# Kernel optimization log

Measured on AMD Instinct MI355X. Metric: run time of the kernel, lower is better.

Reference implementation:

```python
import jax, jax.numpy as jnp
import numpy as np


def _gru_layer(x, W_ih, W_hh, b_ih, b_hh):
    # x: [B, T, in]; W_ih: [3H, in]; W_hh: [3H, H]; gate order (r, z, n) as in PyTorch.
    B, T, _ = x.shape
    H = W_hh.shape[1]
    # Precompute input-side gate pre-activations for the whole sequence (batched GEMM).
    gi = jnp.einsum('bti,gi->btg', x, W_ih) + b_ih  # [B, T, 3H]

    def step(h, gi_t):
        gh = h @ W_hh.T + b_hh                      # [B, 3H]
        i_r, i_z, i_n = jnp.split(gi_t, 3, axis=-1)
        h_r, h_z, h_n = jnp.split(gh, 3, axis=-1)
        r = jax.nn.sigmoid(i_r + h_r)
        z = jax.nn.sigmoid(i_z + h_z)
        n = jnp.tanh(i_n + r * h_n)
        h_new = (1.0 - z) * n + z * h
        return h_new, h_new

    h0 = jnp.zeros((B, H), x.dtype)
    _, hs = jax.lax.scan(step, h0, jnp.swapaxes(gi, 0, 1))  # hs: [T, B, H]
    return jnp.swapaxes(hs, 0, 1)                            # [B, T, H]


def setup_inputs() -> dict:
    key = jax.random.key(0)
    ks = jax.random.split(key, 11)
    B, T, I, H, O = 512, 512, 64, 128, 1
    s = 0.1  # keep gate pre-activations out of saturation
    return {
        'x':     jax.random.normal(ks[0], (B, T, I), jnp.float32),
        'W_ih0': jax.random.normal(ks[1], (3 * H, I), jnp.float32) * s,
        'W_hh0': jax.random.normal(ks[2], (3 * H, H), jnp.float32) * s,
        'b_ih0': jax.random.normal(ks[3], (3 * H,), jnp.float32) * s,
        'b_hh0': jax.random.normal(ks[4], (3 * H,), jnp.float32) * s,
        'W_ih1': jax.random.normal(ks[5], (3 * H, H), jnp.float32) * s,
        'W_hh1': jax.random.normal(ks[6], (3 * H, H), jnp.float32) * s,
        'b_ih1': jax.random.normal(ks[7], (3 * H,), jnp.float32) * s,
        'b_hh1': jax.random.normal(ks[8], (3 * H,), jnp.float32) * s,
        'W_fc':  jax.random.normal(ks[9], (O, H), jnp.float32) * s,
        'b_fc':  jax.random.normal(ks[10], (O,), jnp.float32) * s,
    }


def reference(x, W_ih0, W_hh0, b_ih0, b_hh0, W_ih1, W_hh1, b_ih1, b_hh1, W_fc, b_fc):
    h1 = _gru_layer(x, W_ih0, W_hh0, b_ih0, b_hh0)   # [B, T, H]
    h2 = _gru_layer(h1, W_ih1, W_hh1, b_ih1, b_hh1)  # [B, T, H]
    return h2[:, -1, :] @ W_fc.T + b_fc               # [B, O]
```

## Files before the change

kernel.cpp:

```cpp
#include <hip/hip_runtime.h>
#include <stdint.h>

typedef __bf16 bf16x8 __attribute__((ext_vector_type(8)));
typedef float  floatx4 __attribute__((ext_vector_type(4)));
typedef int    i32x4  __attribute__((ext_vector_type(4)));

#define T_LEN 512
#define BT    4
#define NTHR  1024
#define XS    72
#define HIS   144
#define HFS   132

#if __has_builtin(__builtin_amdgcn_exp2f)
#define EXP2(x) __builtin_amdgcn_exp2f(x)
#else
#define EXP2(x) exp2f(x)
#endif

#define MFMA_BF(a,b,c)  __builtin_amdgcn_mfma_f32_16x16x32_bf16((a),(b),(c),0,0,0)
#define MFMA_I8(a,b,c)  __builtin_amdgcn_mfma_i32_16x16x64_i8((a),(b),(c),0,0,0)

#define BARRIER_LDS() asm volatile("s_waitcnt lgkmcnt(0)\n\ts_barrier" ::: "memory")

#define L2E   1.4426950408889634f
#define S_RZ  (-L2E / (254.f * 127.f))
#define S_N   (-2.f * L2E / (254.f * 127.f))

__device__ __forceinline__ float rcpf(float x) { return __builtin_amdgcn_rcpf(x); }

__device__ __forceinline__ bf16x8 wfrag_bf(const float* W, int ldk, int row, int k0, float scale) {
    const float* p = W + (size_t)row * ldk + k0;
    bf16x8 r;
    #pragma unroll
    for (int j = 0; j < 8; ++j) r[j] = (__bf16)(p[j] * scale);
    return r;
}
__device__ __forceinline__ i32x4 wfrag_i8(const float* W, int ldk, int row, int k0) {
    const float* p = W + (size_t)row * ldk + k0;
    i32x4 r;
    #pragma unroll
    for (int d = 0; d < 4; ++d) {
        uint32_t dw = 0;
        #pragma unroll
        for (int j = 0; j < 4; ++j) {
            float q = __builtin_rintf(p[d * 4 + j] * 254.f);
            q = fminf(127.f, fmaxf(-127.f, q));
            dw |= ((uint32_t)((int)q & 0xff)) << (8 * j);
        }
        r[d] = (int)dw;
    }
    return r;
}

__global__ __launch_bounds__(NTHR, 4) void gru_fused(
    const float* __restrict__ x,
    const float* __restrict__ Wih0, const float* __restrict__ Whh0,
    const float* __restrict__ bih0, const float* __restrict__ bhh0,
    const float* __restrict__ Wih1, const float* __restrict__ Whh1,
    const float* __restrict__ bih1, const float* __restrict__ bhh1,
    const float* __restrict__ Wfc,  const float* __restrict__ bfc,
    float* __restrict__ out)
{
    __shared__ __align__(16) __bf16      xb[2][16 * XS];
    __shared__ __align__(16) signed char h0i[2][16 * HIS];
    __shared__ __align__(16) signed char h1i[2][16 * HIS];
    __shared__ __align__(16) float       hfin[16 * HFS];

    const int tid  = threadIdx.x;
    const int lane = tid & 63;
    const int ln16 = lane & 15;
    const int quad = lane >> 4;
    const int q8   = quad * 8;
    const int q16  = quad * 16;
    const int wave = tid >> 6;
    const int brow = blockIdx.x * BT;

    for (int i = tid; i < 16 * HIS; i += NTHR) {
        h0i[0][i] = 0; h0i[1][i] = 0;
        h1i[0][i] = 0; h1i[1][i] = 0;
    }
    for (int i = tid; i < 16 * XS; i += NTHR) {
        xb[0][i] = (__bf16)0.f; xb[1][i] = (__bf16)0.f;
    }
    __syncthreads();

    if (wave < 8) {
        const int wv = wave;
        const int c  = wv * 16 + ln16;
        const float bNi = -2.f * L2E * bih0[256 + c];
        const float bNh = -2.f * L2E * bhh0[256 + c];
        const float bR  = -L2E * (bih0[c] + bhh0[c]);
        const float bZ  = -L2E * (bih0[128 + c] + bhh0[128 + c]);
        bf16x8 wI[3][2];
        i32x4  wH[3][2];
        #pragma unroll
        for (int g = 0; g < 3; ++g) {
            const int row = g * 128 + c;
            const float sc = (g == 2) ? (-2.f * L2E) : (-L2E);
            #pragma unroll
            for (int q = 0; q < 2; ++q) {
                wI[g][q] = wfrag_bf(Wih0, 64, row, q * 32 + q8, sc);
                wH[g][q] = wfrag_i8(Whh0, 128, row, q * 64 + q16);
            }
        }

        const bool loader = (lane < 32);
        const int lidx = wv * 32 + lane;
        const int sb = (lidx >> 6) & 3, scg = lidx & 63;
        const float* xp = x + (size_t)(brow + sb) * T_LEN * 64 + scg;
        float vxA = 0.f, vxB = 0.f;
        if (loader) {
            xb[0][(sb * 4) * XS + scg] = (__bf16)xp[0];
            xb[1][(sb * 4) * XS + scg] = (__bf16)xp[64];
            vxA = xp[2 * 64];
            vxB = xp[3 * 64];
        }
        __syncthreads();

        float hfv = 0.f;
        floatx4 pR, pZ, pNi;
        {
            bf16x8 ax0 = *(const bf16x8*)&xb[0][ln16 * XS + q8];
            bf16x8 ax1 = *(const bf16x8*)&xb[0][ln16 * XS + 32 + q8];
            floatx4 fR  = {bR, bR, bR, bR};
            floatx4 fZ  = {bZ, bZ, bZ, bZ};
            floatx4 fNi = {bNi, bNi, bNi, bNi};
            fR  = MFMA_BF(ax0, wI[0][0], fR);  fR  = MFMA_BF(ax1, wI[0][1], fR);
            fZ  = MFMA_BF(ax0, wI[1][0], fZ);  fZ  = MFMA_BF(ax1, wI[1][1], fZ);
            fNi = MFMA_BF(ax0, wI[2][0], fNi); fNi = MFMA_BF(ax1, wI[2][1], fNi);
            pR = fR; pZ = fZ; pNi = fNi;
        }

        for (int tt = 0; tt <= T_LEN + 1; ++tt) {
            __builtin_amdgcn_sched_barrier(0);
            BARRIER_LDS();
            if (loader) {
                xb[tt & 1][(sb * 4) * XS + scg] = (__bf16)vxA;
                vxA = vxB;
                int tl = tt + 4; if (tl > T_LEN - 1) tl = T_LEN - 1;
                vxB = xp[(size_t)tl * 64];
            }

            if (tt < T_LEN) {
                const int Rp = (tt + 1) & 1, Wc = tt & 1;
                i32x4 ah[2];
                #pragma unroll
                for (int q = 0; q < 2; ++q)
                    ah[q] = *(const i32x4*)&h0i[Rp][ln16 * HIS + q * 64 + q16];
                i32x4 cR = {0,0,0,0}, cZ = {0,0,0,0}, cNh = {0,0,0,0};
                #pragma unroll
                for (int q = 0; q < 2; ++q) {
                    cR  = MFMA_I8(ah[q], wH[0][q], cR);
                    cZ  = MFMA_I8(ah[q], wH[1][q], cZ);
                    cNh = MFMA_I8(ah[q], wH[2][q], cNh);
                }
                const float pr  = fmaf((float)cR[0],  S_RZ, pR[0]);
                const float pz  = fmaf((float)cZ[0],  S_RZ, pZ[0]);
                const float phn = fmaf((float)cNh[0], S_N,  bNh);
                const float r = rcpf(1.f + EXP2(pr));
                const float z = rcpf(1.f + EXP2(pz));
                const float n = 2.f * rcpf(1.f + EXP2(fmaf(r, phn, pNi[0]))) - 1.f;
                const float h = n + z * (hfv - n);
                hfv = h;
                h0i[Wc][(quad * 4) * HIS + c] =
                    (signed char)(int)__builtin_rintf(h * 127.f);
            }

            if (tt + 1 < T_LEN) {
                const int Rn = (tt + 1) & 1;
                bf16x8 ax0 = *(const bf16x8*)&xb[Rn][ln16 * XS + q8];
                bf16x8 ax1 = *(const bf16x8*)&xb[Rn][ln16 * XS + 32 + q8];
                floatx4 fR  = {bR, bR, bR, bR};
                floatx4 fZ  = {bZ, bZ, bZ, bZ};
                floatx4 fNi = {bNi, bNi, bNi, bNi};
                fR  = MFMA_BF(ax0, wI[0][0], fR);  fR  = MFMA_BF(ax1, wI[0][1], fR);
                fZ  = MFMA_BF(ax0, wI[1][0], fZ);  fZ  = MFMA_BF(ax1, wI[1][1], fZ);
                fNi = MFMA_BF(ax0, wI[2][0], fNi); fNi = MFMA_BF(ax1, wI[2][1], fNi);
                pR = fR; pZ = fZ; pNi = fNi;
            }
        }
    } else {
        const int wv = wave - 8;
        const int c  = wv * 16 + ln16;
        const float bNi1 = -2.f * L2E * bih1[256 + c];
        const float bNh1 = -2.f * L2E * bhh1[256 + c];
        const float bR1  = -L2E * (bih1[c] + bhh1[c]);
        const float bZ1  = -L2E * (bih1[128 + c] + bhh1[128 + c]);
        i32x4 wI[3][2], wH[3][2];
        #pragma unroll
        for (int g = 0; g < 3; ++g) {
            const int row = g * 128 + c;
            #pragma unroll
            for (int q = 0; q < 2; ++q) {
                wI[g][q] = wfrag_i8(Wih1, 128, row, q * 64 + q16);
                wH[g][q] = wfrag_i8(Whh1, 128, row, q * 64 + q16);
            }
        }
        __syncthreads();

        float hfv = 0.f;
        i32x4 pIR, pIZ, pINi;
        for (int tt = 0; tt <= T_LEN + 1; ++tt) {
            __builtin_amdgcn_sched_barrier(0);
            BARRIER_LDS();
            if (tt >= 2) {
                const int Rp = (tt + 1) & 1;
                const int Wc = tt & 1;
                i32x4 a1[2];
                #pragma unroll
                for (int q = 0; q < 2; ++q)
                    a1[q] = *(const i32x4*)&h1i[Rp][ln16 * HIS + q * 64 + q16];
                i32x4 cR = pIR, cZ = pIZ, cNh = {0,0,0,0};
                #pragma unroll
                for (int q = 0; q < 2; ++q) {
                    cR  = MFMA_I8(a1[q], wH[0][q], cR);
                    cZ  = MFMA_I8(a1[q], wH[1][q], cZ);
                    cNh = MFMA_I8(a1[q], wH[2][q], cNh);
                }
                const float pr  = fmaf((float)cR[0],    S_RZ, bR1);
                const float pz  = fmaf((float)cZ[0],    S_RZ, bZ1);
                const float pin = fmaf((float)pINi[0],  S_N,  bNi1);
                const float phn = fmaf((float)cNh[0],   S_N,  bNh1);
                const float r = rcpf(1.f + EXP2(pr));
                const float z = rcpf(1.f + EXP2(pz));
                const float n = 2.f * rcpf(1.f + EXP2(fmaf(r, phn, pin))) - 1.f;
                const float h = n + z * (hfv - n);
                hfv = h;
                h1i[Wc][(quad * 4) * HIS + c] =
                    (signed char)(int)__builtin_rintf(h * 127.f);
            }
            if (tt >= 1 && tt <= T_LEN) {
                const int Rh = (tt + 1) & 1;
                i32x4 ah[2];
                #pragma unroll
                for (int q = 0; q < 2; ++q)
                    ah[q] = *(const i32x4*)&h0i[Rh][ln16 * HIS + q * 64 + q16];
                i32x4 cR = {0,0,0,0}, cZ = {0,0,0,0}, cNi = {0,0,0,0};
                #pragma unroll
                for (int q = 0; q < 2; ++q) {
                    cR  = MFMA_I8(ah[q], wI[0][q], cR);
                    cZ  = MFMA_I8(ah[q], wI[1][q], cZ);
                    cNi = MFMA_I8(ah[q], wI[2][q], cNi);
                }
                pIR = cR; pIZ = cZ; pINi = cNi;
            }
        }
        hfin[(quad * 4) * HFS + c] = hfv;
    }

    __syncthreads();
    {
        const int row = tid >> 5, l = tid & 31;
        if (row < 16 && (row & 3) == 0) {
            float s = 0.f;
            #pragma unroll
            for (int k = 0; k < 4; ++k)
                s += hfin[row * HFS + l + 32 * k] * Wfc[l + 32 * k];
            #pragma unroll
            for (int d = 16; d >= 1; d >>= 1) s += __shfl_down(s, d, 32);
            if (l == 0) out[brow + (row >> 2)] = s + bfc[0];
        }
    }
}

extern "C" void kernel_launch(void* const* d_in, const int* in_sizes, int n_in,
                              void* d_out, int out_size, void* d_ws, size_t ws_size,
                              hipStream_t stream) {
    const float* x    = (const float*)d_in[0];
    const float* Wih0 = (const float*)d_in[1];
    const float* Whh0 = (const float*)d_in[2];
    const float* bih0 = (const float*)d_in[3];
    const float* bhh0 = (const float*)d_in[4];
    const float* Wih1 = (const float*)d_in[5];
    const float* Whh1 = (const float*)d_in[6];
    const float* bih1 = (const float*)d_in[7];
    const float* bhh1 = (const float*)d_in[8];
    const float* Wfc  = (const float*)d_in[9];
    const float* bfc  = (const float*)d_in[10];
    float* out = (float*)d_out;

    hipLaunchKernelGGL(gru_fused, dim3(512 / BT), dim3(NTHR), 0, stream,
                       x, Wih0, Whh0, bih0, bhh0, Wih1, Whh1, bih1, bhh1, Wfc, bfc, out);
}
```

Baseline: 418.7 us.

## Batch input-side GEMMs over groups of four timesteps using unused MFMA rows

The input projection (x for layer 0, h0 for layer 1) now packs four timesteps into the 16 MFMA rows, so each MFMA computes four steps' input gates at once instead of one step per MFMA with only a quarter of the rows used. Layer 1 now lags layer 0 by one four-step group rather than one step, and layer 0 writes its hidden state both to the recurrent buffer and to a new group buffer. This cuts the input-side MFMA and LDS-read work per step by four, at the cost of an extra LDS buffer, an extra store per step, and a pipeline that is four steps longer.

```diff
diff --git a/kernel.cpp b/kernel.cpp
--- a/kernel.cpp
+++ b/kernel.cpp
@@ -6,6 +6,7 @@
 typedef int    i32x4  __attribute__((ext_vector_type(4)));
 
 #define T_LEN 512
+#define NG    (T_LEN / 4)
 #define BT    4
 #define NTHR  1024
 #define XS    72
@@ -62,9 +63,10 @@
     const float* __restrict__ Wfc,  const float* __restrict__ bfc,
     float* __restrict__ out)
 {
-    __shared__ __align__(16) __bf16      xb[2][16 * XS];
-    __shared__ __align__(16) signed char h0i[2][16 * HIS];
-    __shared__ __align__(16) signed char h1i[2][16 * HIS];
+    __shared__ __align__(16) __bf16      xg[2][16 * XS];
+    __shared__ __align__(16) signed char h0b[2][16 * HIS];
+    __shared__ __align__(16) signed char h0g[2][16 * HIS];
+    __shared__ __align__(16) signed char h1b[2][16 * HIS];
     __shared__ __align__(16) float       hfin[16 * HFS];
 
     const int tid  = threadIdx.x;
@@ -77,17 +79,17 @@
     const int brow = blockIdx.x * BT;
 
     for (int i = tid; i < 16 * HIS; i += NTHR) {
-        h0i[0][i] = 0; h0i[1][i] = 0;
-        h1i[0][i] = 0; h1i[1][i] = 0;
+        h0b[0][i] = 0; h0b[1][i] = 0;
+        h0g[0][i] = 0; h0g[1][i] = 0;
+        h1b[0][i] = 0; h1b[1][i] = 0;
     }
     for (int i = tid; i < 16 * XS; i += NTHR) {
-        xb[0][i] = (__bf16)0.f; xb[1][i] = (__bf16)0.f;
+        xg[0][i] = (__bf16)0.f; xg[1][i] = (__bf16)0.f;
     }
     __syncthreads();
 
     if (wave < 8) {
-        const int wv = wave;
-        const int c  = wv * 16 + ln16;
+        const int c = wave * 16 + ln16;
         const float bNi = -2.f * L2E * bih0[256 + c];
         const float bNh = -2.f * L2E * bhh0[256 + c];
         const float bR  = -L2E * (bih0[c] + bhh0[c]);
@@ -106,78 +108,72 @@
         }
 
         const bool loader = (lane < 32);
-        const int lidx = wv * 32 + lane;
+        const int lidx = wave * 32 + lane;
         const int sb = (lidx >> 6) & 3, scg = lidx & 63;
         const float* xp = x + (size_t)(brow + sb) * T_LEN * 64 + scg;
-        float vxA = 0.f, vxB = 0.f;
+        float vx0 = 0.f, vx1 = 0.f, vx2 = 0.f;
         if (loader) {
-            xb[0][(sb * 4) * XS + scg] = (__bf16)xp[0];
-            xb[1][(sb * 4) * XS + scg] = (__bf16)xp[64];
-            vxA = xp[2 * 64];
-            vxB = xp[3 * 64];
+            #pragma unroll
+            for (int tq = 0; tq < 4; ++tq)
+                xg[0][(tq + 4 * sb) * XS + scg] = (__bf16)xp[(size_t)tq * 64];
+            vx0 = xp[4 * 64];
+            vx1 = xp[5 * 64];
+            vx2 = xp[6 * 64];
         }
         __syncthreads();
 
         float hfv = 0.f;
         floatx4 pR, pZ, pNi;
-        {
-            bf16x8 ax0 = *(const bf16x8*)&xb[0][ln16 * XS + q8];
-            bf16x8 ax1 = *(const bf16x8*)&xb[0][ln16 * XS + 32 + q8];
-            floatx4 fR  = {bR, bR, bR, bR};
-            floatx4 fZ  = {bZ, bZ, bZ, bZ};
-            floatx4 fNi = {bNi, bNi, bNi, bNi};
-            fR  = MFMA_BF(ax0, wI[0][0], fR);  fR  = MFMA_BF(ax1, wI[0][1], fR);
-            fZ  = MFMA_BF(ax0, wI[1][0], fZ);  fZ  = MFMA_BF(ax1, wI[1][1], fZ);
-            fNi = MFMA_BF(ax0, wI[2][0], fNi); fNi = MFMA_BF(ax1, wI[2][1], fNi);
-            pR = fR; pZ = fZ; pNi = fNi;
-        }
-
-        for (int tt = 0; tt <= T_LEN + 1; ++tt) {
-            __builtin_amdgcn_sched_barrier(0);
-            BARRIER_LDS();
-            if (loader) {
-                xb[tt & 1][(sb * 4) * XS + scg] = (__bf16)vxA;
-                vxA = vxB;
-                int tl = tt + 4; if (tl > T_LEN - 1) tl = T_LEN - 1;
-                vxB = xp[(size_t)tl * 64];
-            }
-
-            if (tt < T_LEN) {
-                const int Rp = (tt + 1) & 1, Wc = tt & 1;
-                i32x4 ah[2];
-                #pragma unroll
-                for (int q = 0; q < 2; ++q)
-                    ah[q] = *(const i32x4*)&h0i[Rp][ln16 * HIS + q * 64 + q16];
-                i32x4 cR = {0,0,0,0}, cZ = {0,0,0,0}, cNh = {0,0,0,0};
-                #pragma unroll
-                for (int q = 0; q < 2; ++q) {
-                    cR  = MFMA_I8(ah[q], wH[0][q], cR);
-                    cZ  = MFMA_I8(ah[q], wH[1][q], cZ);
-                    cNh = MFMA_I8(ah[q], wH[2][q], cNh);
+        for (int G = 0; G <= NG; ++G) {
+            const bool act = (G < NG);
+            #pragma unroll
+            for (int p = 0; p < 4; ++p) {
+                const int tt = 4 * G + p;
+                __builtin_amdgcn_sched_barrier(0);
+                BARRIER_LDS();
+                if (loader) {
+                    if (tt + 4 < T_LEN)
+                        xg[(G + 1) & 1][(p + 4 * sb) * XS + scg] = (__bf16)vx0;
+                    vx0 = vx1; vx1 = vx2;
+                    int tl = tt + 7; if (tl > T_LEN - 1) tl = T_LEN - 1;
+                    vx2 = xp[(size_t)tl * 64];
                 }
-                const float pr  = fmaf((float)cR[0],  S_RZ, pR[0]);
-                const float pz  = fmaf((float)cZ[0],  S_RZ, pZ[0]);
-                const float phn = fmaf((float)cNh[0], S_N,  bNh);
-                const float r = rcpf(1.f + EXP2(pr));
-                const float z = rcpf(1.f + EXP2(pz));
-                const float n = 2.f * rcpf(1.f + EXP2(fmaf(r, phn, pNi[0]))) - 1.f;
-                const float h = n + z * (hfv - n);
-                hfv = h;
-                h0i[Wc][(quad * 4) * HIS + c] =
-                    (signed char)(int)__builtin_rintf(h * 127.f);
-            }
-
-            if (tt + 1 < T_LEN) {
-                const int Rn = (tt + 1) & 1;
-                bf16x8 ax0 = *(const bf16x8*)&xb[Rn][ln16 * XS + q8];
-                bf16x8 ax1 = *(const bf16x8*)&xb[Rn][ln16 * XS + 32 + q8];
-                floatx4 fR  = {bR, bR, bR, bR};
-                floatx4 fZ  = {bZ, bZ, bZ, bZ};
-                floatx4 fNi = {bNi, bNi, bNi, bNi};
-                fR  = MFMA_BF(ax0, wI[0][0], fR);  fR  = MFMA_BF(ax1, wI[0][1], fR);
-                fZ  = MFMA_BF(ax0, wI[1][0], fZ);  fZ  = MFMA_BF(ax1, wI[1][1], fZ);
-                fNi = MFMA_BF(ax0, wI[2][0], fNi); fNi = MFMA_BF(ax1, wI[2][1], fNi);
-                pR = fR; pZ = fZ; pNi = fNi;
+                if (act) {
+                    if (p == 0) {
+                        bf16x8 ax0 = *(const bf16x8*)&xg[G & 1][ln16 * XS + q8];
+                        bf16x8 ax1 = *(const bf16x8*)&xg[G & 1][ln16 * XS + 32 + q8];
+                        floatx4 fR  = {bR, bR, bR, bR};
+                        floatx4 fZ  = {bZ, bZ, bZ, bZ};
+                        floatx4 fNi = {bNi, bNi, bNi, bNi};
+                        fR  = MFMA_BF(ax0, wI[0][0], fR);  fR  = MFMA_BF(ax1, wI[0][1], fR);
+                        fZ  = MFMA_BF(ax0, wI[1][0], fZ);  fZ  = MFMA_BF(ax1, wI[1][1], fZ);
+                        fNi = MFMA_BF(ax0, wI[2][0], fNi); fNi = MFMA_BF(ax1, wI[2][1], fNi);
+                        pR = fR; pZ = fZ; pNi = fNi;
+                    }
+                    const int Rp = (tt + 1) & 1, Wc = tt & 1;
+                    i32x4 ah[2];
+                    #pragma unroll
+                    for (int q = 0; q < 2; ++q)
+                        ah[q] = *(const i32x4*)&h0b[Rp][ln16 * HIS + q * 64 + q16];
+                    i32x4 cR = {0,0,0,0}, cZ = {0,0,0,0}, cNh = {0,0,0,0};
+                    #pragma unroll
+                    for (int q = 0; q < 2; ++q) {
+                        cR  = MFMA_I8(ah[q], wH[0][q], cR);
+                        cZ  = MFMA_I8(ah[q], wH[1][q], cZ);
+                        cNh = MFMA_I8(ah[q], wH[2][q], cNh);
+                    }
+                    const float pr  = fmaf((float)cR[0],  S_RZ, pR[p]);
+                    const float pz  = fmaf((float)cZ[0],  S_RZ, pZ[p]);
+                    const float phn = fmaf((float)cNh[0], S_N,  bNh);
+                    const float r = rcpf(1.f + EXP2(pr));
+                    const float z = rcpf(1.f + EXP2(pz));
+                    const float n = 2.f * rcpf(1.f + EXP2(fmaf(r, phn, pNi[p]))) - 1.f;
+                    const float h = n + z * (hfv - n);
+                    hfv = h;
+                    const signed char qv = (signed char)(int)__builtin_rintf(h * 127.f);
+                    h0b[Wc][(quad * 4) * HIS + c] = qv;
+                    h0g[G & 1][(p + 4 * quad) * HIS + c] = qv;
+                }
             }
         }
     } else {
@@ -200,50 +196,53 @@
         __syncthreads();
 
         float hfv = 0.f;
-        i32x4 pIR, pIZ, pINi;
-        for (int tt = 0; tt <= T_LEN + 1; ++tt) {
-            __builtin_amdgcn_sched_barrier(0);
-            BARRIER_LDS();
-            if (tt >= 2) {
-                const int Rp = (tt + 1) & 1;
-                const int Wc = tt & 1;
-                i32x4 a1[2];
-                #pragma unroll
-                for (int q = 0; q < 2; ++q)
-                    a1[q] = *(const i32x4*)&h1i[Rp][ln16 * HIS + q * 64 + q16];
-                i32x4 cR = pIR, cZ = pIZ, cNh = {0,0,0,0};
-                #pragma unroll
-                for (int q = 0; q < 2; ++q) {
-                    cR  = MFMA_I8(a1[q], wH[0][q], cR);
-                    cZ  = MFMA_I8(a1[q], wH[1][q], cZ);
-                    cNh = MFMA_I8(a1[q], wH[2][q], cNh);
+        i32x4 gR, gZ, gNi;
+        for (int G = 0; G <= NG; ++G) {
+            const bool act = (G >= 1);
+            #pragma unroll
+            for (int p = 0; p < 4; ++p) {
+                __builtin_amdgcn_sched_barrier(0);
+                BARRIER_LDS();
+                if (act) {
+                    if (p == 0) {
+                        i32x4 ag[2];
+                        #pragma unroll
+                        for (int q = 0; q < 2; ++q)
+                            ag[q] = *(const i32x4*)&h0g[(G - 1) & 1][ln16 * HIS + q * 64 + q16];
+                        i32x4 aR = {0,0,0,0}, aZ = {0,0,0,0}, aN = {0,0,0,0};
+                        #pragma unroll
+                        for (int q = 0; q < 2; ++q) {
+                            aR = MFMA_I8(ag[q], wI[0][q], aR);
+                            aZ = MFMA_I8(ag[q], wI[1][q], aZ);
+                            aN = MFMA_I8(ag[q], wI[2][q], aN);
+                        }
+                        gR = aR; gZ = aZ; gNi = aN;
+                    }
+                    const int s  = 4 * (G - 1) + p;
+                    const int Rp = (s + 1) & 1, Wc = s & 1;
+                    i32x4 a1[2];
+                    #pragma unroll
+                    for (int q = 0; q < 2; ++q)
+                        a1[q] = *(const i32x4*)&h1b[Rp][ln16 * HIS + q * 64 + q16];
+                    i32x4 cR = {0,0,0,0}, cZ = {0,0,0,0}, cNh = {0,0,0,0};
+                    #pragma unroll
+                    for (int q = 0; q < 2; ++q) {
+                        cR  = MFMA_I8(a1[q], wH[0][q], cR);
+                        cZ  = MFMA_I8(a1[q], wH[1][q], cZ);
+                        cNh = MFMA_I8(a1[q], wH[2][q], cNh);
+                    }
+                    const float pr  = fmaf((float)(cR[0] + gR[p]), S_RZ, bR1);
+                    const float pz  = fmaf((float)(cZ[0] + gZ[p]), S_RZ, bZ1);
+                    const float pin = fmaf((float)gNi[p], S_N, bNi1);
+                    const float phn = fmaf((float)cNh[0], S_N, bNh1);
+                    const float r = rcpf(1.f + EXP2(pr));
+                    const float z = rcpf(1.f + EXP2(pz));
+                    const float n = 2.f * rcpf(1.f + EXP2(fmaf(r, phn, pin))) - 1.f;
+                    const float h = n + z * (hfv - n);
+                    hfv = h;
+                    h1b[Wc][(quad * 4) * HIS + c] =
+                        (signed char)(int)__builtin_rintf(h * 127.f);
                 }
-                const float pr  = fmaf((float)cR[0],    S_RZ, bR1);
-                const float pz  = fmaf((float)cZ[0],    S_RZ, bZ1);
-                const float pin = fmaf((float)pINi[0],  S_N,  bNi1);
-                const float phn = fmaf((float)cNh[0],   S_N,  bNh1);
-                const float r = rcpf(1.f + EXP2(pr));
-                const float z = rcpf(1.f + EXP2(pz));
-                const float n = 2.f * rcpf(1.f + EXP2(fmaf(r, phn, pin))) - 1.f;
-                const float h = n + z * (hfv - n);
-                hfv = h;
-                h1i[Wc][(quad * 4) * HIS + c] =
-                    (signed char)(int)__builtin_rintf(h * 127.f);
-            }
-            if (tt >= 1 && tt <= T_LEN) {
-                const int Rh = (tt + 1) & 1;
-                i32x4 ah[2];
-                #pragma unroll
-                for (int q = 0; q < 2; ++q)
-                    ah[q] = *(const i32x4*)&h0i[Rh][ln16 * HIS + q * 64 + q16];
-                i32x4 cR = {0,0,0,0}, cZ = {0,0,0,0}, cNi = {0,0,0,0};
-                #pragma unroll
-                for (int q = 0; q < 2; ++q) {
-                    cR  = MFMA_I8(ah[q], wI[0][q], cR);
-                    cZ  = MFMA_I8(ah[q], wI[1][q], cZ);
-                    cNi = MFMA_I8(ah[q], wI[2][q], cNi);
-                }
-                pIR = cR; pIZ = cZ; pINi = cNi;
             }
         }
         hfin[(quad * 4) * HFS + c] = hfv;
```

Result: faster. 351.3 us (-16.1%).
